# Performance work log

Hardware: AMD Instinct MI355X
Metric: run time of the kernel (lower is better)

The kernel has to match this reference:

```python
import jax, jax.numpy as jnp
import numpy as np

ALPHA, GAMMA = 0.8, 2.0
EDGE_W, BOUND_W, CE_W, POS_W = 1.0, 1.0, 1.0, 1.0


def setup_inputs() -> dict:
    key = jax.random.key(0)
    k1, k2 = jax.random.split(key)
    B, C, H, W = 16, 1, 256, 256
    inputs = jax.random.normal(k1, (B, C, H, W), dtype=jnp.float32)
    # binary GT mask (scipy EDT path assumes a {0,1} mask)
    targets = (jax.random.uniform(k2, (B, C, H, W)) < 0.3).astype(jnp.float32)
    return {"inputs": inputs, "targets": targets}


def _edt_sq(seed):
    """Exact squared Euclidean distance transform of a (H,W) bool grid.
    seed==True pixels have distance 0 (i.e. zeros of scipy's input).
    Separable brute-force: d2(x,y) = min_j [ min_i (f(i,j)+(x-i)^2) + (y-j)^2 ]."""
    H, W = seed.shape
    INF = jnp.float32(H * H + W * W)
    f = jnp.where(seed, 0.0, INF)                              # (H,W)
    ih = jnp.arange(H, dtype=jnp.float32)
    dh = (ih[:, None] - ih[None, :]) ** 2                      # (H,H)
    g = jnp.min(f[None, :, :] + dh[:, :, None], axis=1)       # (H,W)
    iw = jnp.arange(W, dtype=jnp.float32)
    dw = (iw[:, None] - iw[None, :]) ** 2                      # (W,W)
    return jnp.min(g[:, :, None] + dw[None, :, :], axis=1)    # (H,W)


def _compute_sdf(gt):
    """gt: (B,1,H,W) binary. Signed distance: edt(~pos) - edt(pos); 0 if no pos."""
    pos = gt[:, 0] > 0.5                                        # (B,H,W)
    d_out = jnp.sqrt(jax.vmap(_edt_sq)(~pos))                   # dist to pos pixels
    d_in = jnp.sqrt(jax.vmap(_edt_sq)(pos))                     # dist to neg pixels
    sdf = d_out - d_in
    has_pos = jnp.any(pos, axis=(1, 2))[:, None, None]
    return jnp.where(has_pos, sdf, 0.0)[:, None]                # (B,1,H,W)


def _sobel_mag(x):
    """kornia.filters.Sobel: replicate pad, normalized sobel kernels (/8), magnitude."""
    kx = jnp.array([[-1., 0., 1.], [-2., 0., 2.], [-1., 0., 1.]], jnp.float32) / 8.0
    ky = kx.T
    k = jnp.stack([kx, ky])[:, None]                            # (2,1,3,3) OIHW
    xp = jnp.pad(x, ((0, 0), (0, 0), (1, 1), (1, 1)), mode='edge')
    g = jax.lax.conv_general_dilated(xp, k, (1, 1), 'VALID',
                                     dimension_numbers=('NCHW', 'OIHW', 'NCHW'))
    return jnp.sqrt(g[:, 0:1] ** 2 + g[:, 1:2] ** 2 + 1e-6)


def reference(inputs, targets):
    x, t = inputs, targets
    log_p = jax.nn.log_sigmoid(x)
    log_np = jax.nn.log_sigmoid(-x)

    # focal
    bce = -(t * log_p + (1.0 - t) * log_np)
    pt = jnp.exp(-bce)
    focal = jnp.mean(ALPHA * (1.0 - pt) ** GAMMA * bce)

    # edge (L1 on sobel magnitudes)
    edge = jnp.mean(jnp.abs(_sobel_mag(jax.nn.sigmoid(x)) - _sobel_mag(t)))

    # boundary: SDF is computed on CPU/numpy in torch -> non-differentiable constant
    sdf = jax.lax.stop_gradient(_compute_sdf(t))
    boundary = jnp.mean((jax.nn.sigmoid(x) - t) * sdf)

    # weighted BCE with logits (pos_weight)
    ce = jnp.mean(-(POS_W * t * log_p + (1.0 - t) * log_np))

    return focal + EDGE_W * edge + BOUND_W * boundary + CE_W * ce
```

## Files before the change

kernel.cpp:

```cpp
#include <hip/hip_runtime.h>
#include <math.h>

#define BB 16
#define HH 256
#define WW 256
#define NN (BB*HH*WW)
#define SCAN_INIT 300
#define BIGR 100000

static __device__ constexpr float INF_EDT = 131072.0f;

__device__ __forceinline__ float sigmoidf(float v){ return 1.0f/(1.0f+expf(-v)); }
__device__ __forceinline__ float logsigf(float v){
  return fminf(v, 0.0f) - log1pf(expf(-fabsf(v)));
}
__device__ __forceinline__ float min3f(float a, float b, float c){
  return fminf(fminf(a, b), c);
}

__global__ __launch_bounds__(256) void edt_cols_scan(const float* __restrict__ tgt,
                                                     float* __restrict__ gA,
                                                     float* __restrict__ gB,
                                                     int* __restrict__ hp_blk){
  __shared__ unsigned int fwd_s[HH*16];
  __shared__ int lastp_s[16*16], firstp_s[16*16];
  __shared__ int lastn_s[16*16], firstn_s[16*16];
  const int b   = blockIdx.x >> 4;
  const int j0  = (blockIdx.x & 15) << 4;
  const int t   = threadIdx.x;
  const int col = t & 15, seg = t >> 4;
  const int j = j0 + col, r0 = seg << 4;

  int dp = SCAN_INIT, dn = SCAN_INIT;
  int firstp = BIGR, lastp = -BIGR, firstn = BIGR, lastn = -BIGR;
  #pragma unroll 4
  for (int i = 0; i < 16; ++i){
    const int gi = r0 + i;
    const float tv = tgt[(b*HH + gi)*WW + j];
    const bool s = tv > 0.5f;
    dp = s ? 0 : dp + 1;
    dn = s ? dn + 1 : 0;
    if (s){ lastp = gi; if (firstp == BIGR) firstp = gi; }
    else  { lastn = gi; if (firstn == BIGR) firstn = gi; }
    fwd_s[gi*16 + col] = ((unsigned)dp << 16) | (unsigned)dn;
  }
  lastp_s[seg*16+col] = lastp; firstp_s[seg*16+col] = firstp;
  lastn_s[seg*16+col] = lastn; firstn_s[seg*16+col] = firstn;
  __syncthreads();

  int upP=-BIGR, dnP=BIGR, upN=-BIGR, dnN=BIGR, allP=-BIGR, allN=-BIGR;
  #pragma unroll
  for (int s2 = 0; s2 < 16; ++s2){
    const int lp = lastp_s[s2*16+col], fp = firstp_s[s2*16+col];
    const int ln = lastn_s[s2*16+col], fn = firstn_s[s2*16+col];
    allP = max(allP, lp); allN = max(allN, ln);
    if (s2 < seg){ upP = max(upP, lp); upN = max(upN, ln); }
    if (s2 > seg){ dnP = min(dnP, fp); dnN = min(dnN, fn); }
  }
  const bool colp = allP >= 0;
  const bool coln = allN >= 0;
  if (t < 64){
    unsigned long long bal = __ballot(colp);
    if (t == 0) hp_blk[blockIdx.x] = bal ? 1 : 0;
  }

  int bp = SCAN_INIT, bn = SCAN_INIT;
  #pragma unroll 4
  for (int i = 15; i >= 0; --i){
    const int gi = r0 + i;
    const unsigned f = fwd_s[gi*16 + col];
    const int fp = (int)(f >> 16), fn = (int)(f & 0xffffu);
    bp = (fp == 0) ? 0 : bp + 1;
    bn = (fn == 0) ? 0 : bn + 1;
    int Dp = min(min(fp, bp), min(gi - upP, dnP - gi));
    int Dn = min(min(fn, bn), min(gi - upN, dnN - gi));
    Dp = min(Dp, 512); Dn = min(Dn, 512);
    const int o = (b*HH + gi)*WW + j;
    gA[o] = colp ? (float)(Dp*Dp) : INF_EDT;
    gB[o] = coln ? (float)(Dn*Dn) : INF_EDT;
  }
}

__global__ __launch_bounds__(256) void fused_row_k(const float* __restrict__ inp,
    const float* __restrict__ tgt, const float* __restrict__ gA, const float* __restrict__ gB,
    const int* __restrict__ hp_blk, float* __restrict__ part){
  __shared__ __align__(16) float ga_s[4][WW];
  __shared__ __align__(16) float gb_s[4][WW];
  __shared__ __align__(16) float ss[6][WW];
  __shared__ __align__(16) float tt[6][WW];
  __shared__ float red[4];
  const int b  = blockIdx.x >> 6;
  const int x0 = (blockIdx.x & 63) << 2;
  const int t  = threadIdx.x;
  const int g = t >> 6, l = t & 63;

  {
    const int l4 = l << 2;
    const int base = (b*HH + x0 + g)*WW + l4;
    *(float4*)&ga_s[g][l4] = *(const float4*)&gA[base];
    *(float4*)&gb_s[g][l4] = *(const float4*)&gB[base];
    for (int k = g; k < 6; k += 4){
      int gr = x0 - 1 + k; gr = gr < 0 ? 0 : (gr > HH-1 ? HH-1 : gr);
      const float4 xv = *(const float4*)&inp[(b*HH + gr)*WW + l4];
      const float4 tv = *(const float4*)&tgt[(b*HH + gr)*WW + l4];
      float4 sv; sv.x = sigmoidf(xv.x); sv.y = sigmoidf(xv.y);
      sv.z = sigmoidf(xv.z); sv.w = sigmoidf(xv.w);
      *(float4*)&ss[k][l4] = sv;
      *(float4*)&tt[k][l4] = tv;
    }
  }
  __syncthreads();

  int hp_ = 0;
  #pragma unroll
  for (int i = 0; i < 16; ++i) hp_ |= hp_blk[b*16 + i];

  const int y = t;
  const int cm = y ? y-1 : 0, cp = y < WW-1 ? y+1 : WW-1;

  float a0m = ss[0][cm], a0c = ss[0][y], a0p = ss[0][cp];
  float a1m = ss[1][cm], a1c = ss[1][y], a1p = ss[1][cp];
  float b0m = tt[0][cm], b0c = tt[0][y], b0p = tt[0][cp];
  float b1m = tt[1][cm], b1c = tt[1][y], b1p = tt[1][cp];

  float acc = 0.0f;
  #pragma unroll
  for (int r = 0; r < 4; ++r){
    float dpv = ga_s[r][y];
    float dnv = gb_s[r][y];
    int wm = (int)sqrtf(fmaxf(dpv, dnv)) + 1; if (wm > 255) wm = 255;
    for (int dj = 1; dj <= wm; dj += 4){
      #pragma unroll
      for (int u = 0; u < 4; ++u){
        const int d = dj + u;
        const float d2 = (float)(d*d);
        const int jl = (y - d) < 0   ? 0   : y - d;
        const int jr = (y + d) > 255 ? 255 : y + d;
        dpv = min3f(dpv, ga_s[r][jl] + d2, ga_s[r][jr] + d2);
        dnv = min3f(dnv, gb_s[r][jl] + d2, gb_s[r][jr] + d2);
      }
    }
    const float a2m = ss[r+2][cm], a2c = ss[r+2][y], a2p = ss[r+2][cp];
    const float b2m = tt[r+2][cm], b2c = tt[r+2][y], b2p = tt[r+2][cp];
    const float gxs = ((a0p-a0m) + 2.0f*(a1p-a1m) + (a2p-a2m)) * 0.125f;
    const float gys = ((a2m-a0m) + 2.0f*(a2c-a0c) + (a2p-a0p)) * 0.125f;
    const float mags = sqrtf(gxs*gxs + gys*gys + 1e-6f);
    const float gxt = ((b0p-b0m) + 2.0f*(b1p-b1m) + (b2p-b2m)) * 0.125f;
    const float gyt = ((b2m-b0m) + 2.0f*(b2c-b0c) + (b2p-b0p)) * 0.125f;
    const float magt = sqrtf(gxt*gxt + gyt*gyt + 1e-6f);
    acc += fabsf(mags - magt);
    a0m=a1m; a0c=a1c; a0p=a1p; a1m=a2m; a1c=a2c; a1p=a2p;
    b0m=b1m; b0c=b1c; b0p=b1p; b1m=b2m; b1c=b2c; b1p=b2p;

    const float xv = inp[(b*HH + x0 + r)*WW + y];
    const float tv = tt[r+1][y];
    const float sg = ss[r+1][y];
    float sdf = sqrtf(dnv) - sqrtf(dpv);
    sdf = hp_ ? sdf : 0.0f;
    acc += (sg - tv) * sdf;
    const float lp = logsigf(xv);
    const float ln = logsigf(-xv);
    const float bce = -(tv*lp + (1.0f - tv)*ln);
    const float pt = expf(-bce);
    const float om = 1.0f - pt;
    acc += 0.8f * om * om * bce;
    acc += bce;
  }

  #pragma unroll
  for (int o = 32; o > 0; o >>= 1) acc += __shfl_down(acc, o);
  if (l == 0) red[g] = acc;
  __syncthreads();
  if (t == 0) part[blockIdx.x] = red[0]+red[1]+red[2]+red[3];
}

__global__ __launch_bounds__(256) void finalize_k(const float* __restrict__ part,
                                                  float* __restrict__ out){
  __shared__ float red[4];
  const int t = threadIdx.x;
  float s = 0.0f;
  #pragma unroll
  for (int i = t; i < 1024; i += 256) s += part[i];
  #pragma unroll
  for (int o = 32; o > 0; o >>= 1) s += __shfl_down(s, o);
  if ((t & 63) == 0) red[t >> 6] = s;
  __syncthreads();
  if (t == 0) out[0] = (red[0]+red[1]+red[2]+red[3]) * (1.0f/(float)NN);
}

extern "C" void kernel_launch(void* const* d_in, const int* in_sizes, int n_in,
                              void* d_out, int out_size, void* d_ws, size_t ws_size,
                              hipStream_t stream){
  const float* inp = (const float*)d_in[0];
  const float* tgt = (const float*)d_in[1];
  float* out = (float*)d_out;
  float* gA   = (float*)d_ws;
  float* gB   = gA + NN;
  float* part = gB + NN;
  int* hp_blk = (int*)(part + 1024);

  edt_cols_scan<<<BB*16, 256, 0, stream>>>(tgt, gA, gB, hp_blk);
  fused_row_k<<<BB*(HH/4), 256, 0, stream>>>(inp, tgt, gA, gB, hp_blk, part);
  finalize_k<<<1, 256, 0, stream>>>(part, out);
}
```

Before: 86.32 us.

## Fold final reduction into row kernel via last-block atomic counter; pad scan smem

Removes the separate finalize kernel launch. Each row block publishes its partial sum with a release store, then bumps a two-level atomic counter, and the last block to finish reduces all partials and writes the output. The counters are zeroed inside the column-scan kernel. Separately, the shared scan buffer stride is padded from 16 to 17 to reduce LDS bank conflicts. The cost is extra atomics per block and a serial tail reduction in one block, in exchange for one fewer launch.

Result: no change. 87.65 us (+1.5%).

```diff
diff --git a/kernel.cpp b/kernel.cpp
--- a/kernel.cpp
+++ b/kernel.cpp
@@ -7,6 +7,8 @@
 #define NN (BB*HH*WW)
 #define SCAN_INIT 300
 #define BIGR 100000
+#define NBLK 1024
+#define FWS 17
 
 static __device__ constexpr float INF_EDT = 131072.0f;
 
@@ -21,8 +23,9 @@
 __global__ __launch_bounds__(256) void edt_cols_scan(const float* __restrict__ tgt,
                                                      float* __restrict__ gA,
                                                      float* __restrict__ gB,
-                                                     int* __restrict__ hp_blk){
-  __shared__ unsigned int fwd_s[HH*16];
+                                                     int* __restrict__ hp_blk,
+                                                     int* __restrict__ cnt){
+  __shared__ unsigned int fwd_s[HH*FWS];
   __shared__ int lastp_s[16*16], firstp_s[16*16];
   __shared__ int lastn_s[16*16], firstn_s[16*16];
   const int b   = blockIdx.x >> 4;
@@ -30,6 +33,8 @@
   const int t   = threadIdx.x;
   const int col = t & 15, seg = t >> 4;
   const int j = j0 + col, r0 = seg << 4;
+
+  if (blockIdx.x == 0 && t < 65) cnt[t] = 0;
 
   int dp = SCAN_INIT, dn = SCAN_INIT;
   int firstp = BIGR, lastp = -BIGR, firstn = BIGR, lastn = -BIGR;
@@ -42,7 +47,7 @@
     dn = s ? dn + 1 : 0;
     if (s){ lastp = gi; if (firstp == BIGR) firstp = gi; }
     else  { lastn = gi; if (firstn == BIGR) firstn = gi; }
-    fwd_s[gi*16 + col] = ((unsigned)dp << 16) | (unsigned)dn;
+    fwd_s[gi*FWS + col] = ((unsigned)dp << 16) | (unsigned)dn;
   }
   lastp_s[seg*16+col] = lastp; firstp_s[seg*16+col] = firstp;
   lastn_s[seg*16+col] = lastn; firstn_s[seg*16+col] = firstn;
@@ -68,7 +73,7 @@
   #pragma unroll 4
   for (int i = 15; i >= 0; --i){
     const int gi = r0 + i;
-    const unsigned f = fwd_s[gi*16 + col];
+    const unsigned f = fwd_s[gi*FWS + col];
     const int fp = (int)(f >> 16), fn = (int)(f & 0xffffu);
     bp = (fp == 0) ? 0 : bp + 1;
     bn = (fn == 0) ? 0 : bn + 1;
@@ -83,12 +88,14 @@
 
 __global__ __launch_bounds__(256) void fused_row_k(const float* __restrict__ inp,
     const float* __restrict__ tgt, const float* __restrict__ gA, const float* __restrict__ gB,
-    const int* __restrict__ hp_blk, float* __restrict__ part){
+    const int* __restrict__ hp_blk, float* __restrict__ part, int* __restrict__ cnt,
+    float* __restrict__ out){
   __shared__ __align__(16) float ga_s[4][WW];
   __shared__ __align__(16) float gb_s[4][WW];
   __shared__ __align__(16) float ss[6][WW];
   __shared__ __align__(16) float tt[6][WW];
   __shared__ float red[4];
+  __shared__ int winner_s;
   const int b  = blockIdx.x >> 6;
   const int x0 = (blockIdx.x & 63) << 2;
   const int t  = threadIdx.x;
@@ -171,21 +178,30 @@
   for (int o = 32; o > 0; o >>= 1) acc += __shfl_down(acc, o);
   if (l == 0) red[g] = acc;
   __syncthreads();
-  if (t == 0) part[blockIdx.x] = red[0]+red[1]+red[2]+red[3];
-}
-
-__global__ __launch_bounds__(256) void finalize_k(const float* __restrict__ part,
-                                                  float* __restrict__ out){
-  __shared__ float red[4];
-  const int t = threadIdx.x;
-  float s = 0.0f;
-  #pragma unroll
-  for (int i = t; i < 1024; i += 256) s += part[i];
-  #pragma unroll
-  for (int o = 32; o > 0; o >>= 1) s += __shfl_down(s, o);
-  if ((t & 63) == 0) red[t >> 6] = s;
-  __syncthreads();
-  if (t == 0) out[0] = (red[0]+red[1]+red[2]+red[3]) * (1.0f/(float)NN);
+
+  if (t == 0){
+    const float p = red[0]+red[1]+red[2]+red[3];
+    __hip_atomic_store(&part[blockIdx.x], p, __ATOMIC_RELEASE, __HIP_MEMORY_SCOPE_AGENT);
+    int win = 0;
+    const int grp = blockIdx.x >> 4;
+    if (atomicAdd(&cnt[grp], 1) == 15){
+      if (atomicAdd(&cnt[64], 1) == 63) win = 1;
+    }
+    winner_s = win;
+  }
+  __syncthreads();
+
+  if (winner_s){
+    float s = 0.0f;
+    #pragma unroll
+    for (int i = t; i < NBLK; i += 256)
+      s += __hip_atomic_load(&part[i], __ATOMIC_ACQUIRE, __HIP_MEMORY_SCOPE_AGENT);
+    #pragma unroll
+    for (int o = 32; o > 0; o >>= 1) s += __shfl_down(s, o);
+    if (l == 0) red[g] = s;
+    __syncthreads();
+    if (t == 0) out[0] = (red[0]+red[1]+red[2]+red[3]) * (1.0f/(float)NN);
+  }
 }
 
 extern "C" void kernel_launch(void* const* d_in, const int* in_sizes, int n_in,
@@ -197,9 +213,9 @@
   float* gA   = (float*)d_ws;
   float* gB   = gA + NN;
   float* part = gB + NN;
-  int* hp_blk = (int*)(part + 1024);
-
-  edt_cols_scan<<<BB*16, 256, 0, stream>>>(tgt, gA, gB, hp_blk);
-  fused_row_k<<<BB*(HH/4), 256, 0, stream>>>(inp, tgt, gA, gB, hp_blk, part);
-  finalize_k<<<1, 256, 0, stream>>>(part, out);
-}
+  int* hp_blk = (int*)(part + NBLK);
+  int* cnt    = hp_blk + 256;
+
+  edt_cols_scan<<<BB*16, 256, 0, stream>>>(tgt, gA, gB, hp_blk, cnt);
+  fused_row_k<<<NBLK, 256, 0, stream>>>(inp, tgt, gA, gB, hp_blk, part, cnt, out);
+}
```
